# Optimization experiments

Hardware: AMD Instinct MI355X
Metric: run time of the kernel (lower is better)

Reference implementation:

```python
import jax, jax.numpy as jnp
import numpy as np

N_TOKENS = 4096
EMBED = 1024
ATTN = 64


def setup_inputs() -> dict:
    key = jax.random.key(0)
    k1, k2, k3, k4 = jax.random.split(key, 4)
    tokens = jax.random.normal(k1, (N_TOKENS, EMBED), dtype=jnp.float32)
    mask = jnp.ones((1, N_TOKENS), dtype=jnp.float32)
    W_Q = jax.random.uniform(k2, (EMBED, ATTN), dtype=jnp.float32)
    W_K = jax.random.uniform(k3, (EMBED, ATTN), dtype=jnp.float32)
    W_V = jax.random.uniform(k4, (EMBED, ATTN), dtype=jnp.float32)
    return {"tokens": tokens, "mask": mask, "W_Q": W_Q, "W_K": W_K, "W_V": W_V}


def reference(tokens, mask, W_Q, W_K, W_V):
    # Q, K, V: (n_tokens, attn)
    Q = tokens @ W_Q
    K = tokens @ W_K
    V = tokens @ W_V
    scale = jnp.sqrt(jnp.asarray(ATTN, dtype=tokens.dtype))
    # scores: (n_tokens, n_tokens); multiplicative mask then scale, as in source
    scores = (Q @ K.T) * mask
    attn = jax.nn.softmax(scores / scale, axis=1)
    return attn @ V
```

## Files before the change

kernel.cpp:

```cpp
#include <hip/hip_runtime.h>
#include <math.h>

#define NT 4096
#define EMB 1024
#define DH 64
#define PLANE (NT * DH)
#define NSPLIT 16
#define KPS (NT / NSPLIT)
#define KVB 64
#define KSPLIT 8
#define LOG2E 1.44269504088896f

typedef __attribute__((ext_vector_type(8))) short short8;
typedef __attribute__((ext_vector_type(16))) float f32x16;
typedef unsigned short u16;

union U8 { short8 s; uint4 u; unsigned short h[8]; unsigned int w[4]; };

static __device__ __forceinline__ unsigned short f2bf(float x) {
    union { float f; unsigned int u; } v; v.f = x;
    unsigned int r = v.u + 0x7fffu + ((v.u >> 16) & 1u);
    return (unsigned short)(r >> 16);
}
static __device__ __forceinline__ float bf2f(unsigned short h) {
    union { unsigned int u; float f; } v; v.u = ((unsigned int)h) << 16;
    return v.f;
}
static __device__ __forceinline__ unsigned int cvtpk(float a, float b) {
    unsigned int r;
    asm("v_cvt_pk_bf16_f32 %0, %1, %2" : "=v"(r) : "v"(a), "v"(b));
    return r;
}
static __device__ __forceinline__ void split2(float a, float b,
                                              unsigned int& h, unsigned int& lo) {
    h = cvtpk(a, b);
    union { unsigned int u; float f; } ua, ub;
    ua.u = h << 16;
    ub.u = h & 0xffff0000u;
    lo = cvtpk(a - ua.f, b - ub.f);
}

__global__ __launch_bounds__(256) void prep_w(
    const float* __restrict__ wq, const float* __restrict__ wk,
    const float* __restrict__ wv,
    u16* __restrict__ WtSh, u16* __restrict__ WtSl)
{
    int tid = blockIdx.x * 256 + threadIdx.x;
    int col = tid >> 7;
    int ch  = tid & 127;
    const float* W = (col < 64) ? wq : (col < 128) ? wk : wv;
    int wcol = col & 63;
    int k0 = ch * 8;
    float x[8];
#pragma unroll
    for (int i = 0; i < 8; ++i) x[i] = W[(size_t)(k0 + i) * DH + wcol];
    uint4 H, L;
    split2(x[0], x[1], H.x, L.x);
    split2(x[2], x[3], H.y, L.y);
    split2(x[4], x[5], H.z, L.z);
    split2(x[6], x[7], H.w, L.w);
    *(uint4*)&WtSh[(size_t)col * EMB + k0] = H;
    *(uint4*)&WtSl[(size_t)col * EMB + k0] = L;
}

__global__ __launch_bounds__(256) void proj_mfma(
    const float* __restrict__ tokens,
    const u16* __restrict__ WtSh, const u16* __restrict__ WtSl,
    float* __restrict__ part)
{
    __shared__ u16 Th[128][64];
    __shared__ u16 Tl[128][64];
    __shared__ u16 Wh[96][64];
    __shared__ u16 Wl[96][64];

    const int t  = threadIdx.x;
    const int rb = blockIdx.x;
    const int cb = blockIdx.y;
    const int ks = blockIdx.z;
    const int w    = t >> 6;
    const int lane = t & 63;
    const int g    = lane >> 5;
    const int c    = lane & 31;
    const int rowbase = rb * 128;

    f32x16 acc[3];
#pragma unroll
    for (int ct = 0; ct < 3; ++ct)
#pragma unroll
        for (int i = 0; i < 16; ++i) acc[ct][i] = 0.f;

    for (int st = 0; st < 2; ++st) {
        const int kbase = ks * (EMB / KSPLIT) + st * 64;
        __syncthreads();
#pragma unroll
        for (int i = 0; i < 4; ++i) {
            int idx = t + 256 * i;
            int r = idx >> 3;
            int slot = idx & 7;
            const float* gp = tokens + (size_t)(rowbase + r) * EMB + kbase + slot * 8;
            float4 a = *(const float4*)gp;
            float4 b = *(const float4*)(gp + 4);
            uint4 H, L;
            split2(a.x, a.y, H.x, L.x);
            split2(a.z, a.w, H.y, L.y);
            split2(b.x, b.y, H.z, L.z);
            split2(b.z, b.w, H.w, L.w);
            int dst = (slot ^ (r & 7)) * 8;
            *(uint4*)&Th[r][dst] = H;
            *(uint4*)&Tl[r][dst] = L;
        }
#pragma unroll
        for (int i = 0; i < 3; ++i) {
            int idx = t + 256 * i;
            int r = idx >> 3;
            int slot = idx & 7;
            size_t gi = (size_t)(cb * 96 + r) * EMB + kbase + slot * 8;
            int dst = (slot ^ (r & 7)) * 8;
            *(uint4*)&Wh[r][dst] = *(const uint4*)&WtSh[gi];
            *(uint4*)&Wl[r][dst] = *(const uint4*)&WtSl[gi];
        }
        __syncthreads();

#pragma unroll
        for (int kt = 0; kt < 4; ++kt) {
            int sA = kt * 2 + g;
            int offA = ((sA ^ (c & 7)) * 8);
            short8 ah = *(const short8*)&Th[w * 32 + c][offA];
            short8 al = *(const short8*)&Tl[w * 32 + c][offA];
#pragma unroll
            for (int ct = 0; ct < 3; ++ct) {
                short8 bh = *(const short8*)&Wh[ct * 32 + c][offA];
                short8 bl = *(const short8*)&Wl[ct * 32 + c][offA];
                acc[ct] = __builtin_amdgcn_mfma_f32_32x32x16_bf16(ah, bh, acc[ct], 0, 0, 0);
                acc[ct] = __builtin_amdgcn_mfma_f32_32x32x16_bf16(ah, bl, acc[ct], 0, 0, 0);
                acc[ct] = __builtin_amdgcn_mfma_f32_32x32x16_bf16(al, bh, acc[ct], 0, 0, 0);
            }
        }
    }

#pragma unroll
    for (int ct = 0; ct < 3; ++ct)
#pragma unroll
        for (int r = 0; r < 16; ++r) {
            int row_l = (r & 3) + 8 * (r >> 2) + 4 * g;
            part[((size_t)ks * NT + rowbase + w * 32 + row_l) * 192 + cb * 96 + ct * 32 + c]
                = acc[ct][r];
        }
}

__global__ __launch_bounds__(256) void merge_conv(
    const float* __restrict__ part, const float* __restrict__ mask,
    u16* __restrict__ Qhg, u16* __restrict__ Qlg,
    u16* __restrict__ Khg, u16* __restrict__ Klg, u16* __restrict__ Vbg)
{
    int tid = blockIdx.x * 256 + threadIdx.x;
    int row = tid / 24;
    int c8  = tid % 24;
    int colbase = c8 * 8;

    float v[8];
#pragma unroll
    for (int i = 0; i < 8; ++i) v[i] = 0.f;
#pragma unroll
    for (int s = 0; s < KSPLIT; ++s) {
        const float* p = part + ((size_t)s * NT + row) * 192 + colbase;
        float4 a = *(const float4*)p;
        float4 b = *(const float4*)(p + 4);
        v[0] += a.x; v[1] += a.y; v[2] += a.z; v[3] += a.w;
        v[4] += b.x; v[5] += b.y; v[6] += b.z; v[7] += b.w;
    }

    int plane = colbase >> 6;
    int pc = colbase & 63;
    size_t o = (size_t)row * DH + pc;
    if (plane == 0) {
        uint4 H, L;
        split2(v[0], v[1], H.x, L.x);
        split2(v[2], v[3], H.y, L.y);
        split2(v[4], v[5], H.z, L.z);
        split2(v[6], v[7], H.w, L.w);
        *(uint4*)&Qhg[o] = H;
        *(uint4*)&Qlg[o] = L;
    } else if (plane == 1) {
        float mk = mask[row] * 0.125f * LOG2E;
        uint4 H, L;
        split2(v[0] * mk, v[1] * mk, H.x, L.x);
        split2(v[2] * mk, v[3] * mk, H.y, L.y);
        split2(v[4] * mk, v[5] * mk, H.z, L.z);
        split2(v[6] * mk, v[7] * mk, H.w, L.w);
        *(uint4*)&Khg[o] = H;
        *(uint4*)&Klg[o] = L;
    } else {
        uint4 H;
        H.x = cvtpk(v[0], v[1]);
        H.y = cvtpk(v[2], v[3]);
        H.z = cvtpk(v[4], v[5]);
        H.w = cvtpk(v[6], v[7]);
        *(uint4*)&Vbg[o] = H;
    }
}

__global__ __launch_bounds__(256) void attn_mfma(
    const u16* __restrict__ Qhg, const u16* __restrict__ Qlg,
    const u16* __restrict__ Khg, const u16* __restrict__ Klg,
    const u16* __restrict__ Vbg,
    u16* __restrict__ opart, float* __restrict__ mlbuf)
{
    __shared__ u16 Kh[64][64];
    __shared__ u16 Kl[64][64];
    __shared__ unsigned int V2[32][64];

    const int t    = threadIdx.x;
    const int qb   = blockIdx.x;
    const int sp   = blockIdx.y;
    const int wq   = t >> 6;
    const int lane = t & 63;
    const int g    = lane >> 5;
    const int c    = lane & 31;
    const int qrow = qb * 128 + wq * 32 + c;

    short8 qh[4], ql[4];
#pragma unroll
    for (int kt = 0; kt < 4; ++kt) {
        size_t o = (size_t)qrow * DH + kt * 16 + g * 8;
        U8 H, L;
        H.u = *(const uint4*)&Qhg[o];
        L.u = *(const uint4*)&Qlg[o];
        qh[kt] = H.s;
        ql[kt] = L.s;
    }

    f32x16 oa[2];
#pragma unroll
    for (int i = 0; i < 16; ++i) { oa[0][i] = 0.f; oa[1][i] = 0.f; }
    float m = -INFINITY, l = 0.f;

    for (int cb = 0; cb < KPS / KVB; ++cb) {
        const int kv = sp * KPS + cb * KVB;
        __syncthreads();
#pragma unroll
        for (int it = 0; it < 2; ++it) {
            int idx = it * 256 + t;
            int j = idx >> 3, gr = idx & 7;
            int colp = (gr * 8) ^ ((j & 7) * 8);
            *(uint4*)&Kh[j][colp] = *(const uint4*)&Khg[(size_t)(kv + j) * DH + gr * 8];
            *(uint4*)&Kl[j][colp] = *(const uint4*)&Klg[(size_t)(kv + j) * DH + gr * 8];
        }
        {
            int a2 = t >> 3, dg = t & 7;
            uint4 r0 = *(const uint4*)&Vbg[(size_t)(kv + a2 * 2) * DH + dg * 8];
            uint4 r1 = *(const uint4*)&Vbg[(size_t)(kv + a2 * 2 + 1) * DH + dg * 8];
            const unsigned int* p0 = (const unsigned int*)&r0;
            const unsigned int* p1 = (const unsigned int*)&r1;
            unsigned int wv_[8];
#pragma unroll
            for (int i = 0; i < 4; ++i) {
                wv_[2 * i]     = (p0[i] & 0xFFFFu) | (p1[i] << 16);
                wv_[2 * i + 1] = (p0[i] >> 16)     | (p1[i] & 0xFFFF0000u);
            }
            int colp = (dg * 8) ^ ((a2 & 7) * 8);
            *(uint4*)&V2[a2][colp]     = *(uint4*)&wv_[0];
            *(uint4*)&V2[a2][colp + 4] = *(uint4*)&wv_[4];
        }
        __syncthreads();

        f32x16 st0, st1;
#pragma unroll
        for (int i = 0; i < 16; ++i) { st0[i] = 0.f; st1[i] = 0.f; }
#pragma unroll
        for (int kt = 0; kt < 4; ++kt) {
            int colp = ((kt * 2 + g) * 8) ^ ((c & 7) * 8);
            short8 kh0 = *(const short8*)&Kh[c][colp];
            short8 kl0 = *(const short8*)&Kl[c][colp];
            short8 kh1 = *(const short8*)&Kh[32 + c][colp];
            short8 kl1 = *(const short8*)&Kl[32 + c][colp];
            st0 = __builtin_amdgcn_mfma_f32_32x32x16_bf16(kh0, qh[kt], st0, 0, 0, 0);
            st1 = __builtin_amdgcn_mfma_f32_32x32x16_bf16(kh1, qh[kt], st1, 0, 0, 0);
            st0 = __builtin_amdgcn_mfma_f32_32x32x16_bf16(kh0, ql[kt], st0, 0, 0, 0);
            st1 = __builtin_amdgcn_mfma_f32_32x32x16_bf16(kh1, ql[kt], st1, 0, 0, 0);
            st0 = __builtin_amdgcn_mfma_f32_32x32x16_bf16(kl0, qh[kt], st0, 0, 0, 0);
            st1 = __builtin_amdgcn_mfma_f32_32x32x16_bf16(kl1, qh[kt], st1, 0, 0, 0);
        }

        float p[32];
        float pm = -INFINITY;
#pragma unroll
        for (int r = 0; r < 16; ++r) {
            pm = fmaxf(pm, st0[r]);
            pm = fmaxf(pm, st1[r]);
        }
        pm = fmaxf(pm, __shfl_xor(pm, 32));
        float mn = fmaxf(m, pm);
        float f  = exp2f(m - mn);
        float rs = 0.f;
#pragma unroll
        for (int r = 0; r < 16; ++r) { p[r]      = exp2f(st0[r] - mn); rs += p[r]; }
#pragma unroll
        for (int r = 0; r < 16; ++r) { p[16 + r] = exp2f(st1[r] - mn); rs += p[16 + r]; }
        rs += __shfl_xor(rs, 32);
        l = l * f + rs;
        m = mn;

        short8 pa[4];
#pragma unroll
        for (int jt = 0; jt < 2; ++jt) {
            const float* pp = &p[jt * 16];
            unsigned int A1 = cvtpk(pp[0], pp[1]),   B1 = cvtpk(pp[4], pp[5]);
            unsigned int A2 = cvtpk(pp[2], pp[3]),   B2 = cvtpk(pp[6], pp[7]);
            unsigned int A3 = cvtpk(pp[8], pp[9]),   B3 = cvtpk(pp[12], pp[13]);
            unsigned int A4 = cvtpk(pp[10], pp[11]), B4 = cvtpk(pp[14], pp[15]);
            unsigned int xA1 = (unsigned int)__shfl_xor((int)A1, 32);
            unsigned int xB1 = (unsigned int)__shfl_xor((int)B1, 32);
            unsigned int xA2 = (unsigned int)__shfl_xor((int)A2, 32);
            unsigned int xB2 = (unsigned int)__shfl_xor((int)B2, 32);
            unsigned int xA3 = (unsigned int)__shfl_xor((int)A3, 32);
            unsigned int xB3 = (unsigned int)__shfl_xor((int)B3, 32);
            unsigned int xA4 = (unsigned int)__shfl_xor((int)A4, 32);
            unsigned int xB4 = (unsigned int)__shfl_xor((int)B4, 32);
            U8 f0, f1;
            f0.w[0] = g ? xB1 : A1;
            f0.w[1] = g ? xB2 : A2;
            f0.w[2] = g ? B1  : xA1;
            f0.w[3] = g ? B2  : xA2;
            f1.w[0] = g ? xB3 : A3;
            f1.w[1] = g ? xB4 : A4;
            f1.w[2] = g ? B3  : xA3;
            f1.w[3] = g ? B4  : xA4;
            pa[jt * 2]     = f0.s;
            pa[jt * 2 + 1] = f1.s;
        }

#pragma unroll
        for (int r = 0; r < 16; ++r) {
            float fr = __shfl(f, (r & 3) + 8 * (r >> 2) + 4 * g);
            oa[0][r] *= fr;
            oa[1][r] *= fr;
        }

#pragma unroll
        for (int dt = 0; dt < 2; ++dt) {
#pragma unroll
            for (int ksl = 0; ksl < 4; ++ksl) {
                U8 bf;
#pragma unroll
                for (int pq = 0; pq < 4; ++pq) {
                    int j2 = ksl * 8 + g * 4 + pq;
                    int col = (dt * 32 + c) ^ ((j2 & 7) * 8);
                    bf.w[pq] = V2[j2][col];
                }
                oa[dt] = __builtin_amdgcn_mfma_f32_32x32x16_bf16(pa[ksl], bf.s, oa[dt], 0, 0, 0);
            }
        }
    }

    float inv = 1.f / l;
#pragma unroll
    for (int r = 0; r < 16; ++r) {
        int crow = (r & 3) + 8 * (r >> 2) + 4 * g;
        float li = __shfl(inv, crow);
        int row = qb * 128 + wq * 32 + crow;
        size_t o = ((size_t)sp * NT + row) * DH + c;
        opart[o]      = f2bf(oa[0][r] * li);
        opart[o + 32] = f2bf(oa[1][r] * li);
    }
    if (lane < 32) {
        int row = qb * 128 + wq * 32 + lane;
        mlbuf[((size_t)sp * NT + row) * 2 + 0] = m;
        mlbuf[((size_t)sp * NT + row) * 2 + 1] = l;
    }
}

__global__ __launch_bounds__(256) void merge_kernel(
    const u16* __restrict__ opart, const float* __restrict__ mlbuf,
    float* __restrict__ out)
{
    int idx = (blockIdx.x * 256 + threadIdx.x) * 4;
    int row = idx >> 6;
    int d0  = idx & 63;

    float mv[NSPLIT], lv[NSPLIT];
    float mstar = -INFINITY;
#pragma unroll
    for (int s = 0; s < NSPLIT; ++s) {
        mv[s] = mlbuf[((size_t)s * NT + row) * 2 + 0];
        lv[s] = mlbuf[((size_t)s * NT + row) * 2 + 1];
        mstar = fmaxf(mstar, mv[s]);
    }
    float denom = 0.f;
    float ax = 0.f, ay = 0.f, az = 0.f, aw = 0.f;
#pragma unroll
    for (int s = 0; s < NSPLIT; ++s) {
        float w = lv[s] * exp2f(mv[s] - mstar);
        denom += w;
        uint2 ov = *(const uint2*)&opart[((size_t)s * NT + row) * DH + d0];
        ax += w * bf2f((u16)(ov.x & 0xFFFFu));
        ay += w * bf2f((u16)(ov.x >> 16));
        az += w * bf2f((u16)(ov.y & 0xFFFFu));
        aw += w * bf2f((u16)(ov.y >> 16));
    }
    float inv = 1.f / denom;
    *(float4*)&out[idx] = make_float4(ax * inv, ay * inv, az * inv, aw * inv);
}

extern "C" void kernel_launch(void* const* d_in, const int* in_sizes, int n_in,
                              void* d_out, int out_size, void* d_ws, size_t ws_size,
                              hipStream_t stream) {
    const float* tokens = (const float*)d_in[0];
    const float* mask   = (const float*)d_in[1];
    const float* wq     = (const float*)d_in[2];
    const float* wk     = (const float*)d_in[3];
    const float* wv     = (const float*)d_in[4];
    char*  wsb = (char*)d_ws;
    float* out = (float*)d_out;

    u16* WtSh = (u16*)wsb;
    u16* WtSl = WtSh + 192 * EMB;
    u16* Qhg  = WtSl + 192 * EMB;
    u16* Qlg  = Qhg + PLANE;
    u16* Khg  = Qlg + PLANE;
    u16* Klg  = Khg + PLANE;
    u16* Vbg  = Klg + PLANE;
    float* part  = (float*)(wsb + (size_t)4 * 1024 * 1024);
    u16*   opart = (u16*)(wsb + (size_t)4 * 1024 * 1024);
    float* mlbuf = (float*)(wsb + (size_t)28 * 1024 * 1024);

    hipLaunchKernelGGL(prep_w, dim3(96), dim3(256), 0, stream,
                       wq, wk, wv, WtSh, WtSl);
    hipLaunchKernelGGL(proj_mfma, dim3(32, 2, KSPLIT), dim3(256), 0, stream,
                       tokens, WtSh, WtSl, part);
    hipLaunchKernelGGL(merge_conv, dim3(384), dim3(256), 0, stream,
                       part, mask, Qhg, Qlg, Khg, Klg, Vbg);
    hipLaunchKernelGGL(attn_mfma, dim3(NT / 128, NSPLIT), dim3(256), 0, stream,
                       Qhg, Qlg, Khg, Klg, Vbg, opart, mlbuf);
    hipLaunchKernelGGL(merge_kernel, dim3(256), dim3(256), 0, stream,
                       opart, mlbuf, out);
}
```

Baseline: 50.88 us.

## Fuse weight split into projection and double-buffer K/V tiles in attention

Drops the separate prep_w kernel: the projection kernel now reads fp32 weights directly (strided by DH), splits them into bf16 hi/lo pairs and writes them into shared memory. This saves one launch and a workspace round-trip, but every projection block now repeats the weight conversion with uncoalesced strided loads. The attention kernel double-buffers its K/V shared tiles, issuing the next tile's loads before computing on the current one, and uses one barrier per iteration instead of two. The double buffer doubles attention LDS use, which may lower occupancy.

```diff
diff --git a/kernel.cpp b/kernel.cpp
--- a/kernel.cpp
+++ b/kernel.cpp
@@ -40,32 +40,10 @@
     lo = cvtpk(a - ua.f, b - ub.f);
 }
 
-__global__ __launch_bounds__(256) void prep_w(
+__global__ __launch_bounds__(256) void proj_mfma(
+    const float* __restrict__ tokens,
     const float* __restrict__ wq, const float* __restrict__ wk,
     const float* __restrict__ wv,
-    u16* __restrict__ WtSh, u16* __restrict__ WtSl)
-{
-    int tid = blockIdx.x * 256 + threadIdx.x;
-    int col = tid >> 7;
-    int ch  = tid & 127;
-    const float* W = (col < 64) ? wq : (col < 128) ? wk : wv;
-    int wcol = col & 63;
-    int k0 = ch * 8;
-    float x[8];
-#pragma unroll
-    for (int i = 0; i < 8; ++i) x[i] = W[(size_t)(k0 + i) * DH + wcol];
-    uint4 H, L;
-    split2(x[0], x[1], H.x, L.x);
-    split2(x[2], x[3], H.y, L.y);
-    split2(x[4], x[5], H.z, L.z);
-    split2(x[6], x[7], H.w, L.w);
-    *(uint4*)&WtSh[(size_t)col * EMB + k0] = H;
-    *(uint4*)&WtSl[(size_t)col * EMB + k0] = L;
-}
-
-__global__ __launch_bounds__(256) void proj_mfma(
-    const float* __restrict__ tokens,
-    const u16* __restrict__ WtSh, const u16* __restrict__ WtSl,
     float* __restrict__ part)
 {
     __shared__ u16 Th[128][64];
@@ -112,12 +90,22 @@
 #pragma unroll
         for (int i = 0; i < 3; ++i) {
             int idx = t + 256 * i;
-            int r = idx >> 3;
+            int col = idx >> 3;
             int slot = idx & 7;
-            size_t gi = (size_t)(cb * 96 + r) * EMB + kbase + slot * 8;
-            int dst = (slot ^ (r & 7)) * 8;
-            *(uint4*)&Wh[r][dst] = *(const uint4*)&WtSh[gi];
-            *(uint4*)&Wl[r][dst] = *(const uint4*)&WtSl[gi];
+            int colg = cb * 96 + col;
+            const float* W = (colg < 64) ? wq : (colg < 128) ? wk : wv;
+            const float* wp = W + (size_t)(kbase + slot * 8) * DH + (colg & 63);
+            float x[8];
+#pragma unroll
+            for (int j = 0; j < 8; ++j) x[j] = wp[j * DH];
+            uint4 H, L;
+            split2(x[0], x[1], H.x, L.x);
+            split2(x[2], x[3], H.y, L.y);
+            split2(x[4], x[5], H.z, L.z);
+            split2(x[6], x[7], H.w, L.w);
+            int dst = (slot ^ (col & 7)) * 8;
+            *(uint4*)&Wh[col][dst] = H;
+            *(uint4*)&Wl[col][dst] = L;
         }
         __syncthreads();
 
@@ -206,9 +194,9 @@
     const u16* __restrict__ Vbg,
     u16* __restrict__ opart, float* __restrict__ mlbuf)
 {
-    __shared__ u16 Kh[64][64];
-    __shared__ u16 Kl[64][64];
-    __shared__ unsigned int V2[32][64];
+    __shared__ u16 Kh[2][64][64];
+    __shared__ u16 Kl[2][64][64];
+    __shared__ unsigned int V2[2][32][64];
 
     const int t    = threadIdx.x;
     const int qb   = blockIdx.x;
@@ -219,6 +207,33 @@
     const int c    = lane & 31;
     const int qrow = qb * 128 + wq * 32 + c;
 
+    auto stage = [&](int b, int kv) {
+#pragma unroll
+        for (int it = 0; it < 2; ++it) {
+            int idx = it * 256 + t;
+            int j = idx >> 3, gr = idx & 7;
+            int colp = (gr * 8) ^ ((j & 7) * 8);
+            *(uint4*)&Kh[b][j][colp] = *(const uint4*)&Khg[(size_t)(kv + j) * DH + gr * 8];
+            *(uint4*)&Kl[b][j][colp] = *(const uint4*)&Klg[(size_t)(kv + j) * DH + gr * 8];
+        }
+        {
+            int a2 = t >> 3, dg = t & 7;
+            uint4 r0 = *(const uint4*)&Vbg[(size_t)(kv + a2 * 2) * DH + dg * 8];
+            uint4 r1 = *(const uint4*)&Vbg[(size_t)(kv + a2 * 2 + 1) * DH + dg * 8];
+            const unsigned int* p0 = (const unsigned int*)&r0;
+            const unsigned int* p1 = (const unsigned int*)&r1;
+            unsigned int wv_[8];
+#pragma unroll
+            for (int i = 0; i < 4; ++i) {
+                wv_[2 * i]     = (p0[i] & 0xFFFFu) | (p1[i] << 16);
+                wv_[2 * i + 1] = (p0[i] >> 16)     | (p1[i] & 0xFFFF0000u);
+            }
+            int colp = (dg * 8) ^ ((a2 & 7) * 8);
+            *(uint4*)&V2[b][a2][colp]     = *(uint4*)&wv_[0];
+            *(uint4*)&V2[b][a2][colp + 4] = *(uint4*)&wv_[4];
+        }
+    };
+
     short8 qh[4], ql[4];
 #pragma unroll
     for (int kt = 0; kt < 4; ++kt) {
@@ -235,34 +250,12 @@
     for (int i = 0; i < 16; ++i) { oa[0][i] = 0.f; oa[1][i] = 0.f; }
     float m = -INFINITY, l = 0.f;
 
+    stage(0, sp * KPS);
+    __syncthreads();
+
     for (int cb = 0; cb < KPS / KVB; ++cb) {
-        const int kv = sp * KPS + cb * KVB;
-        __syncthreads();
-#pragma unroll
-        for (int it = 0; it < 2; ++it) {
-            int idx = it * 256 + t;
-            int j = idx >> 3, gr = idx & 7;
-            int colp = (gr * 8) ^ ((j & 7) * 8);
-            *(uint4*)&Kh[j][colp] = *(const uint4*)&Khg[(size_t)(kv + j) * DH + gr * 8];
-            *(uint4*)&Kl[j][colp] = *(const uint4*)&Klg[(size_t)(kv + j) * DH + gr * 8];
-        }
-        {
-            int a2 = t >> 3, dg = t & 7;
-            uint4 r0 = *(const uint4*)&Vbg[(size_t)(kv + a2 * 2) * DH + dg * 8];
-            uint4 r1 = *(const uint4*)&Vbg[(size_t)(kv + a2 * 2 + 1) * DH + dg * 8];
-            const unsigned int* p0 = (const unsigned int*)&r0;
-            const unsigned int* p1 = (const unsigned int*)&r1;
-            unsigned int wv_[8];
-#pragma unroll
-            for (int i = 0; i < 4; ++i) {
-                wv_[2 * i]     = (p0[i] & 0xFFFFu) | (p1[i] << 16);
-                wv_[2 * i + 1] = (p0[i] >> 16)     | (p1[i] & 0xFFFF0000u);
-            }
-            int colp = (dg * 8) ^ ((a2 & 7) * 8);
-            *(uint4*)&V2[a2][colp]     = *(uint4*)&wv_[0];
-            *(uint4*)&V2[a2][colp + 4] = *(uint4*)&wv_[4];
-        }
-        __syncthreads();
+        const int cur = cb & 1;
+        if (cb + 1 < KPS / KVB) stage(cur ^ 1, sp * KPS + (cb + 1) * KVB);
 
         f32x16 st0, st1;
 #pragma unroll
@@ -270,10 +263,10 @@
 #pragma unroll
         for (int kt = 0; kt < 4; ++kt) {
             int colp = ((kt * 2 + g) * 8) ^ ((c & 7) * 8);
-            short8 kh0 = *(const short8*)&Kh[c][colp];
-            short8 kl0 = *(const short8*)&Kl[c][colp];
-            short8 kh1 = *(const short8*)&Kh[32 + c][colp];
-            short8 kl1 = *(const short8*)&Kl[32 + c][colp];
+            short8 kh0 = *(const short8*)&Kh[cur][c][colp];
+            short8 kl0 = *(const short8*)&Kl[cur][c][colp];
+            short8 kh1 = *(const short8*)&Kh[cur][32 + c][colp];
+            short8 kl1 = *(const short8*)&Kl[cur][32 + c][colp];
             st0 = __builtin_amdgcn_mfma_f32_32x32x16_bf16(kh0, qh[kt], st0, 0, 0, 0);
             st1 = __builtin_amdgcn_mfma_f32_32x32x16_bf16(kh1, qh[kt], st1, 0, 0, 0);
             st0 = __builtin_amdgcn_mfma_f32_32x32x16_bf16(kh0, ql[kt], st0, 0, 0, 0);
@@ -346,11 +339,12 @@
                 for (int pq = 0; pq < 4; ++pq) {
                     int j2 = ksl * 8 + g * 4 + pq;
                     int col = (dt * 32 + c) ^ ((j2 & 7) * 8);
-                    bf.w[pq] = V2[j2][col];
+                    bf.w[pq] = V2[cur][j2][col];
                 }
                 oa[dt] = __builtin_amdgcn_mfma_f32_32x32x16_bf16(pa[ksl], bf.s, oa[dt], 0, 0, 0);
             }
         }
+        __syncthreads();
     }
 
     float inv = 1.f / l;
@@ -413,9 +407,7 @@
     char*  wsb = (char*)d_ws;
     float* out = (float*)d_out;
 
-    u16* WtSh = (u16*)wsb;
-    u16* WtSl = WtSh + 192 * EMB;
-    u16* Qhg  = WtSl + 192 * EMB;
+    u16* Qhg  = (u16*)wsb;
     u16* Qlg  = Qhg + PLANE;
     u16* Khg  = Qlg + PLANE;
     u16* Klg  = Khg + PLANE;
@@ -424,10 +416,8 @@
     u16*   opart = (u16*)(wsb + (size_t)4 * 1024 * 1024);
     float* mlbuf = (float*)(wsb + (size_t)28 * 1024 * 1024);
 
-    hipLaunchKernelGGL(prep_w, dim3(96), dim3(256), 0, stream,
-                       wq, wk, wv, WtSh, WtSl);
     hipLaunchKernelGGL(proj_mfma, dim3(32, 2, KSPLIT), dim3(256), 0, stream,
-                       tokens, WtSh, WtSl, part);
+                       tokens, wq, wk, wv, part);
     hipLaunchKernelGGL(merge_conv, dim3(384), dim3(256), 0, stream,
                        part, mask, Qhg, Qlg, Khg, Klg, Vbg);
     hipLaunchKernelGGL(attn_mfma, dim3(NT / 128, NSPLIT), dim3(256), 0, stream,
```

Measured after the change: 50.21 us. Within noise of the previous version (-1.3%).

## Retile projection to load tokens once per block and double attention splits

Applied to the files above, without the earlier changes.

The projection kernel now tiles 64 rows by all 192 output columns per block instead of 128 rows by 96 columns. Each token tile is therefore loaded and split into bf16 hi/lo only once rather than twice across column blocks, at the cost of a larger weight tile in shared memory per block. The attention key split count doubles from 16 to 32, giving more blocks for parallelism but twice the partial outputs for the merge kernel to combine. The merge kernel reloads the m/l values in its second loop instead of keeping them in register arrays, to save registers.

```diff
diff --git a/kernel.cpp b/kernel.cpp
--- a/kernel.cpp
+++ b/kernel.cpp
@@ -5,7 +5,7 @@
 #define EMB 1024
 #define DH 64
 #define PLANE (NT * DH)
-#define NSPLIT 16
+#define NSPLIT 32
 #define KPS (NT / NSPLIT)
 #define KVB 64
 #define KSPLIT 8
@@ -68,20 +68,21 @@
     const u16* __restrict__ WtSh, const u16* __restrict__ WtSl,
     float* __restrict__ part)
 {
-    __shared__ u16 Th[128][64];
-    __shared__ u16 Tl[128][64];
-    __shared__ u16 Wh[96][64];
-    __shared__ u16 Wl[96][64];
+    __shared__ u16 Th[64][64];
+    __shared__ u16 Tl[64][64];
+    __shared__ u16 Wh[192][64];
+    __shared__ u16 Wl[192][64];
 
     const int t  = threadIdx.x;
     const int rb = blockIdx.x;
-    const int cb = blockIdx.y;
-    const int ks = blockIdx.z;
+    const int ks = blockIdx.y;
     const int w    = t >> 6;
     const int lane = t & 63;
     const int g    = lane >> 5;
     const int c    = lane & 31;
-    const int rowbase = rb * 128;
+    const int wr   = w & 1;
+    const int wt   = w >> 1;
+    const int rowbase = rb * 64;
 
     f32x16 acc[3];
 #pragma unroll
@@ -93,7 +94,7 @@
         const int kbase = ks * (EMB / KSPLIT) + st * 64;
         __syncthreads();
 #pragma unroll
-        for (int i = 0; i < 4; ++i) {
+        for (int i = 0; i < 2; ++i) {
             int idx = t + 256 * i;
             int r = idx >> 3;
             int slot = idx & 7;
@@ -110,27 +111,26 @@
             *(uint4*)&Tl[r][dst] = L;
         }
 #pragma unroll
-        for (int i = 0; i < 3; ++i) {
+        for (int i = 0; i < 6; ++i) {
             int idx = t + 256 * i;
-            int r = idx >> 3;
+            int col = idx >> 3;
             int slot = idx & 7;
-            size_t gi = (size_t)(cb * 96 + r) * EMB + kbase + slot * 8;
-            int dst = (slot ^ (r & 7)) * 8;
-            *(uint4*)&Wh[r][dst] = *(const uint4*)&WtSh[gi];
-            *(uint4*)&Wl[r][dst] = *(const uint4*)&WtSl[gi];
+            size_t gi = (size_t)col * EMB + kbase + slot * 8;
+            int dst = (slot ^ (col & 7)) * 8;
+            *(uint4*)&Wh[col][dst] = *(const uint4*)&WtSh[gi];
+            *(uint4*)&Wl[col][dst] = *(const uint4*)&WtSl[gi];
         }
         __syncthreads();
 
 #pragma unroll
         for (int kt = 0; kt < 4; ++kt) {
-            int sA = kt * 2 + g;
-            int offA = ((sA ^ (c & 7)) * 8);
-            short8 ah = *(const short8*)&Th[w * 32 + c][offA];
-            short8 al = *(const short8*)&Tl[w * 32 + c][offA];
+            int offA = (((kt * 2 + g) ^ (c & 7)) * 8);
+            short8 ah = *(const short8*)&Th[wr * 32 + c][offA];
+            short8 al = *(const short8*)&Tl[wr * 32 + c][offA];
 #pragma unroll
             for (int ct = 0; ct < 3; ++ct) {
-                short8 bh = *(const short8*)&Wh[ct * 32 + c][offA];
-                short8 bl = *(const short8*)&Wl[ct * 32 + c][offA];
+                short8 bh = *(const short8*)&Wh[wt * 96 + ct * 32 + c][offA];
+                short8 bl = *(const short8*)&Wl[wt * 96 + ct * 32 + c][offA];
                 acc[ct] = __builtin_amdgcn_mfma_f32_32x32x16_bf16(ah, bh, acc[ct], 0, 0, 0);
                 acc[ct] = __builtin_amdgcn_mfma_f32_32x32x16_bf16(ah, bl, acc[ct], 0, 0, 0);
                 acc[ct] = __builtin_amdgcn_mfma_f32_32x32x16_bf16(al, bh, acc[ct], 0, 0, 0);
@@ -143,7 +143,7 @@
 #pragma unroll
         for (int r = 0; r < 16; ++r) {
             int row_l = (r & 3) + 8 * (r >> 2) + 4 * g;
-            part[((size_t)ks * NT + rowbase + w * 32 + row_l) * 192 + cb * 96 + ct * 32 + c]
+            part[((size_t)ks * NT + rowbase + wr * 32 + row_l) * 192 + wt * 96 + ct * 32 + c]
                 = acc[ct][r];
         }
 }
@@ -378,19 +378,18 @@
     int row = idx >> 6;
     int d0  = idx & 63;
 
-    float mv[NSPLIT], lv[NSPLIT];
     float mstar = -INFINITY;
 #pragma unroll
-    for (int s = 0; s < NSPLIT; ++s) {
-        mv[s] = mlbuf[((size_t)s * NT + row) * 2 + 0];
-        lv[s] = mlbuf[((size_t)s * NT + row) * 2 + 1];
-        mstar = fmaxf(mstar, mv[s]);
-    }
+    for (int s = 0; s < NSPLIT; ++s)
+        mstar = fmaxf(mstar, mlbuf[((size_t)s * NT + row) * 2 + 0]);
+
     float denom = 0.f;
     float ax = 0.f, ay = 0.f, az = 0.f, aw = 0.f;
 #pragma unroll
     for (int s = 0; s < NSPLIT; ++s) {
-        float w = lv[s] * exp2f(mv[s] - mstar);
+        float mv = mlbuf[((size_t)s * NT + row) * 2 + 0];
+        float lv = mlbuf[((size_t)s * NT + row) * 2 + 1];
+        float w = lv * exp2f(mv - mstar);
         denom += w;
         uint2 ov = *(const uint2*)&opart[((size_t)s * NT + row) * DH + d0];
         ax += w * bf2f((u16)(ov.x & 0xFFFFu));
@@ -426,7 +425,7 @@
 
     hipLaunchKernelGGL(prep_w, dim3(96), dim3(256), 0, stream,
                        wq, wk, wv, WtSh, WtSl);
-    hipLaunchKernelGGL(proj_mfma, dim3(32, 2, KSPLIT), dim3(256), 0, stream,
+    hipLaunchKernelGGL(proj_mfma, dim3(64, KSPLIT), dim3(256), 0, stream,
                        tokens, WtSh, WtSl, part);
     hipLaunchKernelGGL(merge_conv, dim3(384), dim3(256), 0, stream,
                        part, mask, Qhg, Qlg, Khg, Klg, Vbg);
```

New measurement: 52.94 us. 1.04x slower.
